# Performance work log

Hardware: AMD Instinct MI355X
Metric: run time of the kernel (lower is better)

The kernel has to match this reference:

```python
import jax, jax.numpy as jnp
import numpy as np

B, S, D, T = 64, 128, 512, 64  # batch, encoder len, dim_model, longest_coor

def setup_inputs() -> dict:
    key = jax.random.key(0)
    ks = jax.random.split(key, 10)
    def rn(k, shape, s=0.02):
        return jax.random.normal(k, shape, dtype=jnp.float32) * s
    return dict(
        e_all=jax.random.normal(ks[0], (B, S, D), dtype=jnp.float32),
        e_last=jax.random.normal(ks[1], (1, B, D), dtype=jnp.float32),
        Wa_w=rn(ks[2], (D, D)), Wa_b=jnp.zeros((D,), jnp.float32),
        Ua_w=rn(ks[3], (D, D)), Ua_b=jnp.zeros((D,), jnp.float32),
        Va_w=rn(ks[4], (D, 1)), Va_b=jnp.zeros((1,), jnp.float32),
        W_ih=rn(ks[5], (3 * D, D + 3)),  # GRU input weights, input = cat(attn[D], coord[3])
        W_hh=rn(ks[6], (3 * D, D)),
        b_ih=jnp.zeros((3 * D,), jnp.float32),
        b_hh=jnp.zeros((3 * D,), jnp.float32),
        Wo_w=rn(ks[7], (D, 3)), Wo_b=jnp.zeros((3,), jnp.float32),
    )

def reference(e_all, e_last, Wa_w, Wa_b, Ua_w, Ua_b, Va_w, Va_b,
              W_ih, W_hh, b_ih, b_hh, Wo_w, Wo_b):
    # Ua(keys) is step-invariant: hoist out of the decode loop (same math).
    Uk = e_all @ Ua_w + Ua_b                      # [B,S,D]
    h0 = e_last[0]                                # [B,D]
    x0 = jnp.zeros((e_all.shape[0], 3), e_all.dtype)

    def step(carry, _):
        h, x = carry
        # Bahdanau attention: query = current hidden state
        q = h @ Wa_w + Wa_b                       # [B,D]
        scores = jnp.squeeze(jnp.tanh(q[:, None, :] + Uk) @ Va_w, -1) + Va_b  # [B,S]
        w = jax.nn.softmax(scores, axis=-1)       # [B,S]
        ctx = jnp.einsum('bs,bsd->bd', w, e_all)  # [B,D]
        # single-step GRU, input = cat(context, prev coord)
        gin = jnp.concatenate([ctx, x], axis=-1)  # [B,D+3]
        gi = gin @ W_ih.T + b_ih                  # [B,3D]
        gh = h @ W_hh.T + b_hh                    # [B,3D]
        gir, giz, gin_n = jnp.split(gi, 3, axis=-1)
        ghr, ghz, ghn = jnp.split(gh, 3, axis=-1)
        r = jax.nn.sigmoid(gir + ghr)
        z = jax.nn.sigmoid(giz + ghz)
        n = jnp.tanh(gin_n + r * ghn)
        h_new = (1.0 - z) * n + z * h             # [B,D]
        out = h_new @ Wo_w + Wo_b                 # [B,3]
        return (h_new, out), (out, w)

    (hT, _), (outs, attns) = jax.lax.scan(step, (h0, x0), None, length=T)
    d_outputs = jnp.transpose(outs, (1, 0, 2))    # [B,T,3]
    cross_attn = jnp.transpose(attns, (1, 0, 2))  # [B,T,S]
    return d_outputs, hT[None], cross_attn
```

## Files before the change

### kernel.cpp

```cpp
#include <hip/hip_runtime.h>

typedef unsigned int u32;
typedef unsigned long long u64;
typedef float f32x4 __attribute__((ext_vector_type(4)));
typedef short short8 __attribute__((ext_vector_type(8)));

#define OFF_UKB 0u
#define OFF_ECB 8388608u
#define OFF_QX  16777216u
#define OFF_EX  17563648u
#define G_BYTES 73728u

#define OFF_OUT_HT  12288u
#define OFF_OUT_ATT 45056u

#define NBLK 192
#define NTHR 512
#define DYN_LDS 145408
#define PREP_LDS 36864

__device__ __forceinline__ float fast_rcp(float x) { return __builtin_amdgcn_rcpf(x); }
__device__ __forceinline__ float tanh5(float x) {
    float e = __expf(2.f * x);
    return 1.f - 2.f * fast_rcp(e + 1.f);
}
__device__ __forceinline__ float sigm_f(float x) { return fast_rcp(1.f + __expf(-x)); }

__device__ __forceinline__ u32 packbf2(float a, float b) {
    u32 ua = __float_as_uint(a); ua += 0x7FFFu + ((ua >> 16) & 1u);
    u32 ub = __float_as_uint(b); ub += 0x7FFFu + ((ub >> 16) & 1u);
    return (ua >> 16) | (ub & 0xFFFF0000u);
}
__device__ __forceinline__ float2 unpackbf2(u32 u) {
    return make_float2(__uint_as_float(u << 16), __uint_as_float(u & 0xFFFF0000u));
}
__device__ __forceinline__ float bf16hi(float x, float& lo) {
    u32 u = __float_as_uint(x); u += 0x7FFFu + ((u >> 16) & 1u); u &= 0xFFFF0000u;
    const float h = __uint_as_float(u); lo = x - h; return h;
}

__device__ __forceinline__ u64 cload64(const u64* p) {
    return __hip_atomic_load(p, __ATOMIC_RELAXED, __HIP_MEMORY_SCOPE_AGENT);
}
__device__ __forceinline__ void cstore64(u64* p, u64 v) {
    __hip_atomic_store(p, v, __ATOMIC_RELAXED, __HIP_MEMORY_SCOPE_AGENT);
}
__device__ __forceinline__ u32 cload32(const u32* p) {
    return __hip_atomic_load(p, __ATOMIC_RELAXED, __HIP_MEMORY_SCOPE_AGENT);
}
__device__ __forceinline__ void cstore32(u32* p, u32 v) {
    __hip_atomic_store(p, v, __ATOMIC_RELAXED, __HIP_MEMORY_SCOPE_AGENT);
}

union U8 { u32 u[4]; uint4 q; short8 s; };

__global__ __launch_bounds__(256) void prep_kernel(
    const float* __restrict__ e_all, const float* __restrict__ e_last,
    const float* __restrict__ Ua_w,  const float* __restrict__ Ua_b,
    float* __restrict__ ws)
{
    extern __shared__ char pls[];
    u32* Ahi = (u32*)pls;
    u32* Alo = Ahi + 64 * 36;
    u32* Bhi = Alo + 64 * 36;
    u32* Blo = Bhi + 64 * 36;

    u32* UKB = (u32*)((char*)ws + OFF_UKB);

    const int blk = blockIdx.x, tid = threadIdx.x;
    const int gtid = blk * 256 + tid, gstride = 1024 * 256;

    for (int i = gtid; i < 5120; i += gstride) {
        const int g = i / 1280, j = i - g * 1280;
        ((u32*)((char*)ws + OFF_EX + (size_t)g * G_BYTES + 65536))[j] = 0u;
    }
    for (int i = gtid; i < 8192; i += gstride) {
        const int g = i >> 11, i2 = i & 2047;
        const float* ep = e_last + ((size_t)(g * 16 + (i2 >> 7)) * 512) + 4 * (i2 & 127);
        u64* HX = (u64*)((char*)ws + OFF_EX + (size_t)g * G_BYTES);
        HX[i2] = (u64)packbf2(ep[0], ep[1]) | ((u64)packbf2(ep[2], ep[3]) << 32);
    }

    const int r0 = (blk >> 3) * 64, c0 = (blk & 7) * 64;
    const int lane = tid & 63, wv = tid >> 6;
    const int mn = lane & 15, quad = lane >> 4;

    f32x4 acc[4];
    #pragma unroll
    for (int rg = 0; rg < 4; ++rg) acc[rg] = (f32x4){0.f, 0.f, 0.f, 0.f};

    for (int ks = 0; ks < 8; ++ks) {
        if (ks) __syncthreads();
        for (int i = tid; i < 1024; i += 256) {
            const int row = i >> 4, q4i = i & 15;
            const float4 e = *(const float4*)(e_all + (size_t)(r0 + row) * 512 + ks * 64 + 4 * q4i);
            float l0, l1, l2, l3;
            const float h0 = bf16hi(e.x, l0), h1 = bf16hi(e.y, l1);
            const float h2 = bf16hi(e.z, l2), h3 = bf16hi(e.w, l3);
            Ahi[row * 36 + 2 * q4i]     = packbf2(h0, h1);
            Ahi[row * 36 + 2 * q4i + 1] = packbf2(h2, h3);
            Alo[row * 36 + 2 * q4i]     = packbf2(l0, l1);
            Alo[row * 36 + 2 * q4i + 1] = packbf2(l2, l3);
        }
        for (int i = tid; i < 2048; i += 256) {
            const int col = i & 63, kp = i >> 6;
            const float b0 = Ua_w[(size_t)(ks * 64 + 2 * kp) * 512 + c0 + col];
            const float b1 = Ua_w[(size_t)(ks * 64 + 2 * kp + 1) * 512 + c0 + col];
            float l0, l1;
            const float h0 = bf16hi(b0, l0), h1 = bf16hi(b1, l1);
            Bhi[col * 36 + kp] = packbf2(h0, h1);
            Blo[col * 36 + kp] = packbf2(l0, l1);
        }
        __syncthreads();
        #pragma unroll
        for (int kb = 0; kb < 2; ++kb) {
            const int fo = kb * 16 + quad * 4;
            U8 bh, bl;
            bh.q = *(const uint4*)(Bhi + (wv * 16 + mn) * 36 + fo);
            bl.q = *(const uint4*)(Blo + (wv * 16 + mn) * 36 + fo);
            #pragma unroll
            for (int rg = 0; rg < 4; ++rg) {
                U8 ah, al;
                ah.q = *(const uint4*)(Ahi + (rg * 16 + mn) * 36 + fo);
                al.q = *(const uint4*)(Alo + (rg * 16 + mn) * 36 + fo);
                acc[rg] = __builtin_amdgcn_mfma_f32_16x16x32_bf16(al.s, bh.s, acc[rg], 0, 0, 0);
                acc[rg] = __builtin_amdgcn_mfma_f32_16x16x32_bf16(ah.s, bl.s, acc[rg], 0, 0, 0);
                acc[rg] = __builtin_amdgcn_mfma_f32_16x16x32_bf16(ah.s, bh.s, acc[rg], 0, 0, 0);
            }
        }
    }
    const int col = c0 + wv * 16 + mn;
    const float bias = Ua_b[col];
    #pragma unroll
    for (int rg = 0; rg < 4; ++rg) {
        #pragma unroll
        for (int reg = 0; reg < 4; ++reg) {
            const float v = acc[rg][reg] + bias;
            const float v1 = __shfl_down(v, 1);
            if (!(mn & 1))
                UKB[(size_t)(r0 + rg * 16 + quad * 4 + reg) * 256 + (col >> 1)] = packbf2(v, v1);
        }
    }
}

__global__ __launch_bounds__(512, 1) void decode_kernel(
    const float* __restrict__ e_all,
    const float* __restrict__ e_last,
    const float* __restrict__ Wa_w,  const float* __restrict__ Wa_b,
    const float* __restrict__ Va_w,
    const float* __restrict__ W_ih,  const float* __restrict__ W_hh,
    const float* __restrict__ b_ih,  const float* __restrict__ b_hh,
    const float* __restrict__ Wo_w,  const float* __restrict__ Wo_b,
    float* __restrict__ out, float* __restrict__ ws)
{
    extern __shared__ char smraw[];

    const u32* UKB = (const u32*)((char*)ws + OFF_UKB);

    const int tid = threadIdx.x;
    const int bi  = blockIdx.x;
    const int g   = bi / 48, r = bi % 48;
    const int lane = tid & 63, wv = tid >> 6;

    char* gbase = (char*)ws + OFF_EX + (size_t)g * G_BYTES;
    u64* HX = (u64*)gbase;
    u64* CX = (u64*)(gbase + 32768);
    u32* FH = (u32*)(gbase + 65536);
    u32* FC = (u32*)(gbase + 67584);
    u32* FQ = (u32*)(gbase + 68608);

    if (r < 16) {
        const int bl = r, b = g * 16 + bl;
        u32*   EuL  = (u32*)smraw;
        float* eq_s = (float*)(smraw + 131072);
        float* w_s  = (float*)(smraw + 133120);
        float* red  = (float*)(smraw + 133632);
        float* psq  = (float*)(smraw + 133696);

        const u64* QXR = (const u64*)((char*)ws + OFF_QX + (size_t)g * 65536);

        {
            const uint4* src = (const uint4*)(UKB + (size_t)b * 32768);
            uint4* dst = (uint4*)EuL;
            #pragma unroll
            for (int i = 0; i < 16; ++i) {
                uint4 u = src[tid + 512 * i];
                float2 p;
                p = unpackbf2(u.x); u.x = packbf2(__expf(2.f * p.x), __expf(2.f * p.y));
                p = unpackbf2(u.y); u.y = packbf2(__expf(2.f * p.x), __expf(2.f * p.y));
                p = unpackbf2(u.z); u.z = packbf2(__expf(2.f * p.x), __expf(2.f * p.y));
                p = unpackbf2(u.w); u.w = packbf2(__expf(2.f * p.x), __expf(2.f * p.y));
                dst[tid + 512 * i] = u;
            }
        }
        uint2 ereg[32];
        {
            const int dq = tid & 127, sg = tid >> 7;
            const float* ep = e_all + (size_t)b * 65536;
            #pragma unroll
            for (int si = 0; si < 32; ++si) {
                const float4 e = *(const float4*)(ep + (size_t)(sg * 32 + si) * 512 + 4 * dq);
                ereg[si] = make_uint2(packbf2(e.x, e.y), packbf2(e.z, e.w));
            }
        }
        const int kl = lane & 15;
        float4 va2a[4], va2b[4];
        float vaSum = 0.f;
        #pragma unroll
        for (int it = 0; it < 4; ++it) {
            const float4 a  = *(const float4*)(Va_w + (it * 16 + kl) * 8);
            const float4 b2 = *(const float4*)(Va_w + (it * 16 + kl) * 8 + 4);
            vaSum += a.x + a.y + a.z + a.w + b2.x + b2.y + b2.z + b2.w;
            va2a[it] = make_float4(-2.f * a.x,  -2.f * a.y,  -2.f * a.z,  -2.f * a.w);
            va2b[it] = make_float4(-2.f * b2.x, -2.f * b2.y, -2.f * b2.z, -2.f * b2.w);
        }
        __syncthreads();

        for (int t = 0; t < 64; ++t) {
            const int slot = t & 1;
            u64* CxS = CX + slot * 2048;
            const u64* QxS = QXR + slot * 4096;

            if (tid < 256) {
                if (lane < 8) {
                    const u32* f = FQ + (wv * 8 + lane) * 16;
                    while (cload32(f) < (u32)(t + 1)) {}
                }
                const u64 v = cload64(QxS + bl * 256 + tid);
                const float q0 = __uint_as_float((u32)v);
                const float q1 = __uint_as_float((u32)(v >> 32));
                ((float2*)eq_s)[tid] = make_float2(__expf(2.f * q0), __expf(2.f * q1));
            }
            __syncthreads();

            {
                float4 eqa[4], eqb[4];
                const float4* q4 = (const float4*)eq_s;
                #pragma unroll
                for (int it = 0; it < 4; ++it) {
                    eqa[it] = q4[(it * 16 + kl) * 2];  eqb[it] = q4[(it * 16 + kl) * 2 + 1];
                }
                const int sbase = wv * 16 + (lane >> 4);
                #pragma unroll
                for (int sg = 0; sg < 4; ++sg) {
                    const int s = sbase + sg * 4;
                    const uint4* uk4 = (const uint4*)EuL + (size_t)s * 64;
                    float acc = vaSum;
                    #pragma unroll
                    for (int it = 0; it < 4; ++it) {
                        const uint4 u = uk4[it * 16 + kl];
                        const float2 u0 = unpackbf2(u.x), u1 = unpackbf2(u.y);
                        const float2 u2 = unpackbf2(u.z), u3 = unpackbf2(u.w);
                        acc = fmaf(va2a[it].x, fast_rcp(fmaf(eqa[it].x, u0.x, 1.f)), acc);
                        acc = fmaf(va2a[it].y, fast_rcp(fmaf(eqa[it].y, u0.y, 1.f)), acc);
                        acc = fmaf(va2a[it].z, fast_rcp(fmaf(eqa[it].z, u1.x, 1.f)), acc);
                        acc = fmaf(va2a[it].w, fast_rcp(fmaf(eqa[it].w, u1.y, 1.f)), acc);
                        acc = fmaf(va2b[it].x, fast_rcp(fmaf(eqb[it].x, u2.x, 1.f)), acc);
                        acc = fmaf(va2b[it].y, fast_rcp(fmaf(eqb[it].y, u2.y, 1.f)), acc);
                        acc = fmaf(va2b[it].z, fast_rcp(fmaf(eqb[it].z, u3.x, 1.f)), acc);
                        acc = fmaf(va2b[it].w, fast_rcp(fmaf(eqb[it].w, u3.y, 1.f)), acc);
                    }
                    acc += __shfl_xor(acc, 1); acc += __shfl_xor(acc, 2);
                    acc += __shfl_xor(acc, 4); acc += __shfl_xor(acc, 8);
                    if (kl == 0) w_s[s] = __expf(acc);
                }
            }
            __syncthreads();

            if (tid < 64) {
                float sm = w_s[tid] + w_s[tid + 64];
                #pragma unroll
                for (int off = 32; off > 0; off >>= 1) sm += __shfl_down(sm, off);
                if (tid == 0) red[1] = fast_rcp(sm);
            }
            {
                const int dq = tid & 127, sg = tid >> 7;
                float4 a = {0.f, 0.f, 0.f, 0.f};
                #pragma unroll
                for (int si = 0; si < 32; ++si) {
                    const float wgt = w_s[sg * 32 + si];
                    const float2 e0 = unpackbf2(ereg[si].x), e1 = unpackbf2(ereg[si].y);
                    a.x = fmaf(wgt, e0.x, a.x);
                    a.y = fmaf(wgt, e0.y, a.y);
                    a.z = fmaf(wgt, e1.x, a.z);
                    a.w = fmaf(wgt, e1.y, a.w);
                }
                ((float4*)psq)[sg * 128 + dq] = a;
            }
            __syncthreads();
            if (tid < 128) {
                const float rn = red[1];
                const float4* p4 = (const float4*)psq;
                float4 a = p4[tid], b2 = p4[128 + tid], c2 = p4[256 + tid], d2 = p4[384 + tid];
                const float rx = (a.x + b2.x + c2.x + d2.x) * rn;
                const float ry = (a.y + b2.y + c2.y + d2.y) * rn;
                const float rz = (a.z + b2.z + c2.z + d2.z) * rn;
                const float rw = (a.w + b2.w + c2.w + d2.w) * rn;
                cstore64(CxS + bl * 128 + tid,
                         (u64)packbf2(rx, ry) | ((u64)packbf2(rz, rw) << 32));
            }
            __syncthreads();
            if (tid == 0) cstore32(FC + bl * 16, (u32)(t + 1));
            else if (tid >= 128 && tid < 256)
                out[OFF_OUT_ATT + ((size_t)b * 64 + t) * 128 + (tid - 128)] = w_s[tid - 128] * red[1];
        }
    } else {
        const int idx = r - 16, d0 = idx * 16;
        u32*   hbu  = (u32*)smraw;
        u32*   cbu  = (u32*)(smraw + 16640);
        float* gh_s = (float*)(smraw + 33280);
        float* gi_s = (float*)(smraw + 36352);
        float* x_s  = (float*)(smraw + 39424);
        float* wx_s = (float*)(smraw + 39616);
        float* wo_s = (float*)(smraw + 40192);

        u64* QXW = (u64*)((char*)ws + OFF_QX + (size_t)g * 65536);

        const int mn = lane & 15, quad = lane >> 4;

        short8 bfrag[16];
        float qbias = 0.f;
        if (wv < 3) {
            const float* wrow = W_hh + (size_t)(wv * 512 + d0 + mn) * 512;
            #pragma unroll
            for (int kb = 0; kb < 16; ++kb) {
                const int k0 = kb * 32 + quad * 8;
                U8 tpk;
                #pragma unroll
                for (int c = 0; c < 4; ++c)
                    tpk.u[c] = packbf2(wrow[k0 + 2 * c], wrow[k0 + 2 * c + 1]);
                bfrag[kb] = tpk.s;
            }
        } else if (wv < 6) {
            const float* wrow = W_ih + (size_t)((wv - 3) * 512 + d0 + mn) * 515;
            #pragma unroll
            for (int kb = 0; kb < 16; ++kb) {
                const int k0 = kb * 32 + quad * 8;
                U8 tpk;
                #pragma unroll
                for (int c = 0; c < 4; ++c)
                    tpk.u[c] = packbf2(wrow[k0 + 2 * c], wrow[k0 + 2 * c + 1]);
                bfrag[kb] = tpk.s;
            }
        } else if (wv == 6) {
            #pragma unroll
            for (int kb = 0; kb < 16; ++kb) {
                const int k0 = kb * 32 + quad * 8;
                U8 tpk;
                #pragma unroll
                for (int c = 0; c < 4; ++c)
                    tpk.u[c] = packbf2(Wa_w[(size_t)(k0 + 2 * c) * 512 + d0 + mn],
                                       Wa_w[(size_t)(k0 + 2 * c + 1) * 512 + d0 + mn]);
                bfrag[kb] = tpk.s;
            }
            qbias = Wa_b[d0 + mn];
        }
        if (tid < 144) {
            const int dd = tid / 9, rem = tid - dd * 9, g3 = rem / 3, c = rem - g3 * 3;
            wx_s[tid] = W_ih[(size_t)(g3 * 512 + d0 + dd) * 515 + 512 + c];
        }
        for (int i = tid; i < 1536; i += 512) wo_s[i] = Wo_w[i];
        if (tid < 3) wo_s[1536 + tid] = Wo_b[tid];

        const int gb = tid >> 4, gd = tid & 15;
        float hold = 0.f, bih[3], bhh[3];
        if (tid < 256) {
            hold = e_last[(size_t)(g * 16 + gb) * 512 + d0 + gd];
            #pragma unroll
            for (int g3 = 0; g3 < 3; ++g3) {
                bih[g3] = b_ih[g3 * 512 + d0 + gd];
                bhh[g3] = b_hh[g3 * 512 + d0 + gd];
            }
        }

        for (int t = 0; t < 64; ++t) {
            const int slot = t & 1;
            const u64* HxS = HX + slot * 2048;
            const u64* CxS = CX + slot * 2048;
            u64* HxW = HX + ((t + 1) & 1) * 2048;

            if (lane < 16) {
                const u32* f = FH + ((wv & 1) * 16 + lane) * 16;
                while (cload32(f) < (u32)t) {}
            }
            #pragma unroll
            for (int u = 0; u < 4; ++u) {
                const int i = tid + 512 * u;
                const u64 v = cload64(HxS + i);
                *(u64*)(hbu + (i >> 7) * 260 + (i & 127) * 2) = v;
            }
            __syncthreads();

            if (wv < 3) {
                f32x4 c = {0.f, 0.f, 0.f, 0.f};
                #pragma unroll
                for (int kb = 0; kb < 16; ++kb) {
                    U8 a; a.q = *(const uint4*)(hbu + mn * 260 + kb * 16 + quad * 4);
                    c = __builtin_amdgcn_mfma_f32_16x16x32_bf16(a.s, bfrag[kb], c, 0, 0, 0);
                }
                #pragma unroll
                for (int reg = 0; reg < 4; ++reg)
                    gh_s[((quad * 4 + reg) * 16 + mn) * 3 + wv] = c[reg];
            } else if (wv < 6) {
                if (lane < 16) { const u32* f = FC + lane * 16; while (cload32(f) < (u32)(t + 1)) {} }
                const int thr = (wv - 3) * 64 + lane;
                for (int i = thr; i < 2048; i += 192) {
                    const u64 v = cload64(CxS + i);
                    *(u64*)(cbu + (i >> 7) * 260 + (i & 127) * 2) = v;
                }
            } else if (wv == 6) {
                f32x4 c = {0.f, 0.f, 0.f, 0.f};
                #pragma unroll
                for (int kb = 0; kb < 16; ++kb) {
                    U8 a; a.q = *(const uint4*)(hbu + mn * 260 + kb * 16 + quad * 4);
                    c = __builtin_amdgcn_mfma_f32_16x16x32_bf16(a.s, bfrag[kb], c, 0, 0, 0);
                }
                u64* QxW = QXW + slot * 4096;
                #pragma unroll
                for (int reg = 0; reg < 4; ++reg) {
                    const float q0 = c[reg] + qbias;
                    const float q1 = __shfl_down(q0, 1);
                    if ((mn & 1) == 0)
                        cstore64(QxW + (size_t)(quad * 4 + reg) * 256 + idx * 8 + (mn >> 1),
                                 (u64)__float_as_uint(q0) | ((u64)__float_as_uint(q1) << 32));
                }
                asm volatile("s_waitcnt vmcnt(0)" ::: "memory");
                if (lane == 0) cstore32(FQ + idx * 16, (u32)(t + 1));
            } else {
                const int tt = tid - 448, cb = tt >> 2, kl = tt & 3;
                if (t > 0) {
                    float a0 = 0.f, a1 = 0.f, a2 = 0.f;
                    #pragma unroll 4
                    for (int c = 0; c < 64; ++c) {
                        const int p = kl * 64 + c;
                        const float2 hv = unpackbf2(hbu[cb * 260 + p]);
                        const float* w0 = wo_s + 2 * p * 3;
                        a0 = fmaf(hv.x, w0[0], fmaf(hv.y, w0[3], a0));
                        a1 = fmaf(hv.x, w0[1], fmaf(hv.y, w0[4], a1));
                        a2 = fmaf(hv.x, w0[2], fmaf(hv.y, w0[5], a2));
                    }
                    a0 += __shfl_xor(a0, 1); a1 += __shfl_xor(a1, 1); a2 += __shfl_xor(a2, 1);
                    a0 += __shfl_xor(a0, 2); a1 += __shfl_xor(a1, 2); a2 += __shfl_xor(a2, 2);
                    if (kl == 0) {
                        x_s[cb * 3 + 0] = a0 + wo_s[1536];
                        x_s[cb * 3 + 1] = a1 + wo_s[1537];
                        x_s[cb * 3 + 2] = a2 + wo_s[1538];
                    }
                } else if (tt < 48) x_s[tt] = 0.f;
            }
            __syncthreads();

            if (wv >= 3 && wv < 6) {
                f32x4 c = {0.f, 0.f, 0.f, 0.f};
                #pragma unroll
                for (int kb = 0; kb < 16; ++kb) {
                    U8 a; a.q = *(const uint4*)(cbu + mn * 260 + kb * 16 + quad * 4);
                    c = __builtin_amdgcn_mfma_f32_16x16x32_bf16(a.s, bfrag[kb], c, 0, 0, 0);
                }
                #pragma unroll
                for (int reg = 0; reg < 4; ++reg)
                    gi_s[((quad * 4 + reg) * 16 + mn) * 3 + (wv - 3)] = c[reg];
            } else if (idx == 0 && t > 0 && tid < 48) {
                out[((size_t)(g * 16 + tid / 3) * 64 + (t - 1)) * 3 + tid % 3] = x_s[tid];
            }
            __syncthreads();

            if (tid < 256) {
                const int ob = (gb * 16 + gd) * 3;
                const float x0 = x_s[gb * 3 + 0], x1 = x_s[gb * 3 + 1], x2 = x_s[gb * 3 + 2];
                const float giR = gi_s[ob + 0] + bih[0]
                                + x0 * wx_s[gd * 9 + 0] + x1 * wx_s[gd * 9 + 1] + x2 * wx_s[gd * 9 + 2];
                const float giZ = gi_s[ob + 1] + bih[1]
                                + x0 * wx_s[gd * 9 + 3] + x1 * wx_s[gd * 9 + 4] + x2 * wx_s[gd * 9 + 5];
                const float giN = gi_s[ob + 2] + bih[2]
                                + x0 * wx_s[gd * 9 + 6] + x1 * wx_s[gd * 9 + 7] + x2 * wx_s[gd * 9 + 8];
                const float ghR = gh_s[ob + 0] + bhh[0];
                const float ghZ = gh_s[ob + 1] + bhh[1];
                const float ghN = gh_s[ob + 2] + bhh[2];
                const float rg = sigm_f(giR + ghR);
                const float zg = sigm_f(giZ + ghZ);
                const float ng = tanh5(giN + rg * ghN);
                const float hnew = (1.f - zg) * ng + zg * hold;
                hold = hnew;
                const float s1 = __shfl_down(hnew, 1);
                const float s2 = __shfl_down(hnew, 2);
                const float s3 = __shfl_down(hnew, 3);
                if ((gd & 3) == 0)
                    cstore64(HxW + gb * 128 + ((d0 + gd) >> 2),
                             (u64)packbf2(hnew, s1) | ((u64)packbf2(s2, s3) << 32));
                if (t == 63)
                    out[OFF_OUT_HT + (size_t)(g * 16 + gb) * 512 + d0 + gd] = hnew;
            }
            __syncthreads();
            if (tid == 0) cstore32(FH + idx * 16, (u32)(t + 1));
        }

        if (tid < 32) { const u32* f = FH + tid * 16; while (cload32(f) < 64u) {} }
        __syncthreads();
        #pragma unroll
        for (int u = 0; u < 4; ++u) {
            const int i = tid + 512 * u;
            const u64 v = cload64(HX + i);
            *(u64*)(hbu + (i >> 7) * 260 + (i & 127) * 2) = v;
        }
        __syncthreads();
        if (wv >= 6) {
            const int tt = tid - 384, cb = tt >> 3, kl = tt & 7;
            float a0 = 0.f, a1 = 0.f, a2 = 0.f;
            #pragma unroll 4
            for (int c = 0; c < 32; ++c) {
                const int p = kl * 32 + c;
                const float2 hv = unpackbf2(hbu[cb * 260 + p]);
                const float* w0 = wo_s + 2 * p * 3;
                a0 = fmaf(hv.x, w0[0], fmaf(hv.y, w0[3], a0));
                a1 = fmaf(hv.x, w0[1], fmaf(hv.y, w0[4], a1));
                a2 = fmaf(hv.x, w0[2], fmaf(hv.y, w0[5], a2));
            }
            a0 += __shfl_xor(a0, 1); a1 += __shfl_xor(a1, 1); a2 += __shfl_xor(a2, 1);
            a0 += __shfl_xor(a0, 2); a1 += __shfl_xor(a1, 2); a2 += __shfl_xor(a2, 2);
            a0 += __shfl_xor(a0, 4); a1 += __shfl_xor(a1, 4); a2 += __shfl_xor(a2, 4);
            if (kl == 0) {
                x_s[cb * 3 + 0] = a0 + wo_s[1536];
                x_s[cb * 3 + 1] = a1 + wo_s[1537];
                x_s[cb * 3 + 2] = a2 + wo_s[1538];
            }
        }
        __syncthreads();
        if (idx == 0 && tid < 48)
            out[((size_t)(g * 16 + tid / 3) * 64 + 63) * 3 + tid % 3] = x_s[tid];
    }
}

extern "C" void kernel_launch(void* const* d_in, const int* in_sizes, int n_in,
                              void* d_out, int out_size, void* d_ws, size_t ws_size,
                              hipStream_t stream) {
    const float* e_all  = (const float*)d_in[0];
    const float* e_last = (const float*)d_in[1];
    const float* Wa_w   = (const float*)d_in[2];
    const float* Wa_b   = (const float*)d_in[3];
    const float* Ua_w   = (const float*)d_in[4];
    const float* Ua_b   = (const float*)d_in[5];
    const float* Va_w   = (const float*)d_in[6];
    const float* W_ih   = (const float*)d_in[8];
    const float* W_hh   = (const float*)d_in[9];
    const float* b_ih   = (const float*)d_in[10];
    const float* b_hh   = (const float*)d_in[11];
    const float* Wo_w   = (const float*)d_in[12];
    const float* Wo_b   = (const float*)d_in[13];
    float* outp = (float*)d_out;
    float* ws   = (float*)d_ws;

    hipFuncSetAttribute((const void*)prep_kernel,
                        hipFuncAttributeMaxDynamicSharedMemorySize, PREP_LDS);
    hipFuncSetAttribute((const void*)decode_kernel,
                        hipFuncAttributeMaxDynamicSharedMemorySize, DYN_LDS);

    hipLaunchKernelGGL(prep_kernel, dim3(1024), dim3(256), PREP_LDS, stream,
                       e_all, e_last, Ua_w, Ua_b, ws);

    void* args[] = { (void*)&e_all, (void*)&e_last, (void*)&Wa_w, (void*)&Wa_b,
                     (void*)&Va_w,
                     (void*)&W_ih, (void*)&W_hh, (void*)&b_ih, (void*)&b_hh,
                     (void*)&Wo_w, (void*)&Wo_b, (void*)&outp, (void*)&ws };
    hipError_t err = hipLaunchCooperativeKernel((void*)decode_kernel, dim3(NBLK), dim3(NTHR),
                                                args, DYN_LDS, stream);
    if (err != hipSuccess) {
        hipLaunchKernelGGL(decode_kernel, dim3(NBLK), dim3(NTHR), DYN_LDS, stream,
                           e_all, e_last, Wa_w, Wa_b, Va_w,
                           W_ih, W_hh, b_ih, b_hh, Wo_w, Wo_b, outp, ws);
    }
}
```

Before: 955.3 us.

## Fuse Ua key projection into decode kernel and drop prep launch

```diff
diff --git a/kernel.cpp b/kernel.cpp
--- a/kernel.cpp
+++ b/kernel.cpp
@@ -1,12 +1,11 @@
 #include <hip/hip_runtime.h>
+#include <hip/hip_cooperative_groups.h>
 
 typedef unsigned int u32;
 typedef unsigned long long u64;
 typedef float f32x4 __attribute__((ext_vector_type(4)));
 typedef short short8 __attribute__((ext_vector_type(8)));
 
-#define OFF_UKB 0u
-#define OFF_ECB 8388608u
 #define OFF_QX  16777216u
 #define OFF_EX  17563648u
 #define G_BYTES 73728u
@@ -17,7 +16,6 @@
 #define NBLK 192
 #define NTHR 512
 #define DYN_LDS 145408
-#define PREP_LDS 36864
 
 __device__ __forceinline__ float fast_rcp(float x) { return __builtin_amdgcn_rcpf(x); }
 __device__ __forceinline__ float tanh5(float x) {
@@ -54,92 +52,14 @@
 
 union U8 { u32 u[4]; uint4 q; short8 s; };
 
-__global__ __launch_bounds__(256) void prep_kernel(
-    const float* __restrict__ e_all, const float* __restrict__ e_last,
-    const float* __restrict__ Ua_w,  const float* __restrict__ Ua_b,
-    float* __restrict__ ws)
-{
-    extern __shared__ char pls[];
-    u32* Ahi = (u32*)pls;
-    u32* Alo = Ahi + 64 * 36;
-    u32* Bhi = Alo + 64 * 36;
-    u32* Blo = Bhi + 64 * 36;
-
-    u32* UKB = (u32*)((char*)ws + OFF_UKB);
-
-    const int blk = blockIdx.x, tid = threadIdx.x;
-    const int gtid = blk * 256 + tid, gstride = 1024 * 256;
-
-    for (int i = gtid; i < 5120; i += gstride) {
-        const int g = i / 1280, j = i - g * 1280;
-        ((u32*)((char*)ws + OFF_EX + (size_t)g * G_BYTES + 65536))[j] = 0u;
-    }
-    for (int i = gtid; i < 8192; i += gstride) {
-        const int g = i >> 11, i2 = i & 2047;
-        const float* ep = e_last + ((size_t)(g * 16 + (i2 >> 7)) * 512) + 4 * (i2 & 127);
-        u64* HX = (u64*)((char*)ws + OFF_EX + (size_t)g * G_BYTES);
-        HX[i2] = (u64)packbf2(ep[0], ep[1]) | ((u64)packbf2(ep[2], ep[3]) << 32);
-    }
-
-    const int r0 = (blk >> 3) * 64, c0 = (blk & 7) * 64;
-    const int lane = tid & 63, wv = tid >> 6;
-    const int mn = lane & 15, quad = lane >> 4;
-
-    f32x4 acc[4];
-    #pragma unroll
-    for (int rg = 0; rg < 4; ++rg) acc[rg] = (f32x4){0.f, 0.f, 0.f, 0.f};
-
-    for (int ks = 0; ks < 8; ++ks) {
-        if (ks) __syncthreads();
-        for (int i = tid; i < 1024; i += 256) {
-            const int row = i >> 4, q4i = i & 15;
-            const float4 e = *(const float4*)(e_all + (size_t)(r0 + row) * 512 + ks * 64 + 4 * q4i);
-            float l0, l1, l2, l3;
-            const float h0 = bf16hi(e.x, l0), h1 = bf16hi(e.y, l1);
-            const float h2 = bf16hi(e.z, l2), h3 = bf16hi(e.w, l3);
-            Ahi[row * 36 + 2 * q4i]     = packbf2(h0, h1);
-            Ahi[row * 36 + 2 * q4i + 1] = packbf2(h2, h3);
-            Alo[row * 36 + 2 * q4i]     = packbf2(l0, l1);
-            Alo[row * 36 + 2 * q4i + 1] = packbf2(l2, l3);
-        }
-        for (int i = tid; i < 2048; i += 256) {
-            const int col = i & 63, kp = i >> 6;
-            const float b0 = Ua_w[(size_t)(ks * 64 + 2 * kp) * 512 + c0 + col];
-            const float b1 = Ua_w[(size_t)(ks * 64 + 2 * kp + 1) * 512 + c0 + col];
-            float l0, l1;
-            const float h0 = bf16hi(b0, l0), h1 = bf16hi(b1, l1);
-            Bhi[col * 36 + kp] = packbf2(h0, h1);
-            Blo[col * 36 + kp] = packbf2(l0, l1);
-        }
-        __syncthreads();
-        #pragma unroll
-        for (int kb = 0; kb < 2; ++kb) {
-            const int fo = kb * 16 + quad * 4;
-            U8 bh, bl;
-            bh.q = *(const uint4*)(Bhi + (wv * 16 + mn) * 36 + fo);
-            bl.q = *(const uint4*)(Blo + (wv * 16 + mn) * 36 + fo);
-            #pragma unroll
-            for (int rg = 0; rg < 4; ++rg) {
-                U8 ah, al;
-                ah.q = *(const uint4*)(Ahi + (rg * 16 + mn) * 36 + fo);
-                al.q = *(const uint4*)(Alo + (rg * 16 + mn) * 36 + fo);
-                acc[rg] = __builtin_amdgcn_mfma_f32_16x16x32_bf16(al.s, bh.s, acc[rg], 0, 0, 0);
-                acc[rg] = __builtin_amdgcn_mfma_f32_16x16x32_bf16(ah.s, bl.s, acc[rg], 0, 0, 0);
-                acc[rg] = __builtin_amdgcn_mfma_f32_16x16x32_bf16(ah.s, bh.s, acc[rg], 0, 0, 0);
-            }
-        }
-    }
-    const int col = c0 + wv * 16 + mn;
-    const float bias = Ua_b[col];
-    #pragma unroll
-    for (int rg = 0; rg < 4; ++rg) {
-        #pragma unroll
-        for (int reg = 0; reg < 4; ++reg) {
-            const float v = acc[rg][reg] + bias;
-            const float v1 = __shfl_down(v, 1);
-            if (!(mn & 1))
-                UKB[(size_t)(r0 + rg * 16 + quad * 4 + reg) * 256 + (col >> 1)] = packbf2(v, v1);
-        }
+__global__ __launch_bounds__(256) void flagzero_kernel(float* __restrict__ ws) {
+    const int tid = threadIdx.x;
+    for (int i = tid; i < 320; i += 256) {
+        const int g = i / 80, j = i - g * 80;
+        char* gb = (char*)ws + OFF_EX + (size_t)g * G_BYTES;
+        if (j < 32)      ((u32*)(gb + 65536))[j * 16] = 0u;
+        else if (j < 48) ((u32*)(gb + 67584))[(j - 32) * 16] = 0u;
+        else             ((u32*)(gb + 68608))[(j - 48) * 16] = 0u;
     }
 }
 
@@ -148,14 +68,13 @@
     const float* __restrict__ e_last,
     const float* __restrict__ Wa_w,  const float* __restrict__ Wa_b,
     const float* __restrict__ Va_w,
+    const float* __restrict__ Ua_w,  const float* __restrict__ Ua_b,
     const float* __restrict__ W_ih,  const float* __restrict__ W_hh,
     const float* __restrict__ b_ih,  const float* __restrict__ b_hh,
     const float* __restrict__ Wo_w,  const float* __restrict__ Wo_b,
-    float* __restrict__ out, float* __restrict__ ws)
+    float* __restrict__ out, float* __restrict__ ws, int fused)
 {
     extern __shared__ char smraw[];
-
-    const u32* UKB = (const u32*)((char*)ws + OFF_UKB);
 
     const int tid = threadIdx.x;
     const int bi  = blockIdx.x;
@@ -168,6 +87,15 @@
     u32* FH = (u32*)(gbase + 65536);
     u32* FC = (u32*)(gbase + 67584);
     u32* FQ = (u32*)(gbase + 68608);
+
+    if (fused) {
+        if (tid == 0) {
+            if (r < 16) cstore32(FC + r * 16, 0u);
+            else { cstore32(FH + (r - 16) * 16, 0u); cstore32(FQ + (r - 16) * 16, 0u); }
+        }
+        __threadfence();
+        cooperative_groups::this_grid().sync();
+    }
 
     if (r < 16) {
         const int bl = r, b = g * 16 + bl;
@@ -178,21 +106,92 @@
         float* psq  = (float*)(smraw + 133696);
 
         const u64* QXR = (const u64*)((char*)ws + OFF_QX + (size_t)g * 65536);
+        const int mn = lane & 15, quad = lane >> 4;
 
         {
-            const uint4* src = (const uint4*)(UKB + (size_t)b * 32768);
-            uint4* dst = (uint4*)EuL;
-            #pragma unroll
-            for (int i = 0; i < 16; ++i) {
-                uint4 u = src[tid + 512 * i];
-                float2 p;
-                p = unpackbf2(u.x); u.x = packbf2(__expf(2.f * p.x), __expf(2.f * p.y));
-                p = unpackbf2(u.y); u.y = packbf2(__expf(2.f * p.x), __expf(2.f * p.y));
-                p = unpackbf2(u.z); u.z = packbf2(__expf(2.f * p.x), __expf(2.f * p.y));
-                p = unpackbf2(u.w); u.w = packbf2(__expf(2.f * p.x), __expf(2.f * p.y));
-                dst[tid + 512 * i] = u;
-            }
-        }
+            u32* Ahi = EuL;
+            u32* Alo = Ahi + 4096;
+            u32* Bhi = Alo + 4096;
+            u32* Blo = Bhi + 4096;
+            const float* eb = e_all + (size_t)b * 65536;
+
+            auto run_chunk = [&](int cc, f32x4* acc) {
+                #pragma unroll
+                for (int ct = 0; ct < 8; ++ct) acc[ct] = (f32x4){0.f, 0.f, 0.f, 0.f};
+                for (int kc = 0; kc < 8; ++kc) {
+                    __syncthreads();
+                    for (int i = tid; i < 2048; i += 512) {
+                        const int row = i >> 4, q4 = i & 15;
+                        const float4 e = *(const float4*)(eb + (size_t)row * 512 + kc * 64 + 4 * q4);
+                        float l0, l1, l2, l3;
+                        const float h0 = bf16hi(e.x, l0), h1 = bf16hi(e.y, l1);
+                        const float h2 = bf16hi(e.z, l2), h3 = bf16hi(e.w, l3);
+                        const int sw = (row & 7) << 2;
+                        const int k0 = 2 * q4, k1 = 2 * q4 + 1;
+                        const int a0 = row * 32 + (((k0 & ~3) ^ sw) | (k0 & 3));
+                        const int a1 = row * 32 + (((k1 & ~3) ^ sw) | (k1 & 3));
+                        Ahi[a0] = packbf2(h0, h1); Ahi[a1] = packbf2(h2, h3);
+                        Alo[a0] = packbf2(l0, l1); Alo[a1] = packbf2(l2, l3);
+                    }
+                    for (int i = tid; i < 4096; i += 512) {
+                        const int col = i & 127, kp = i >> 7;
+                        const float b0 = Ua_w[(size_t)(kc * 64 + 2 * kp) * 512 + cc * 128 + col];
+                        const float b1 = Ua_w[(size_t)(kc * 64 + 2 * kp + 1) * 512 + cc * 128 + col];
+                        float l0, l1;
+                        const float h0 = bf16hi(b0, l0), h1 = bf16hi(b1, l1);
+                        const int sw = (col & 7) << 2;
+                        const int ad = col * 32 + (((kp & ~3) ^ sw) | (kp & 3));
+                        Bhi[ad] = packbf2(h0, h1);
+                        Blo[ad] = packbf2(l0, l1);
+                    }
+                    __syncthreads();
+                    #pragma unroll
+                    for (int kb = 0; kb < 2; ++kb) {
+                        const int arow = wv * 16 + mn;
+                        const int fo = (kb * 16 + quad * 4) ^ ((mn & 7) << 2);
+                        U8 ah, al;
+                        ah.q = *(const uint4*)(Ahi + arow * 32 + fo);
+                        al.q = *(const uint4*)(Alo + arow * 32 + fo);
+                        #pragma unroll
+                        for (int ct = 0; ct < 8; ++ct) {
+                            const int bcol = ct * 16 + mn;
+                            U8 bh, bl;
+                            bh.q = *(const uint4*)(Bhi + bcol * 32 + fo);
+                            bl.q = *(const uint4*)(Blo + bcol * 32 + fo);
+                            acc[ct] = __builtin_amdgcn_mfma_f32_16x16x32_bf16(al.s, bh.s, acc[ct], 0, 0, 0);
+                            acc[ct] = __builtin_amdgcn_mfma_f32_16x16x32_bf16(ah.s, bl.s, acc[ct], 0, 0, 0);
+                            acc[ct] = __builtin_amdgcn_mfma_f32_16x16x32_bf16(ah.s, bh.s, acc[ct], 0, 0, 0);
+                        }
+                    }
+                }
+            };
+            auto write_chunk = [&](int cc, f32x4* acc) {
+                #pragma unroll
+                for (int ct = 0; ct < 8; ++ct) {
+                    const float bias = Ua_b[cc * 128 + ct * 16 + mn];
+                    #pragma unroll
+                    for (int reg = 0; reg < 4; ++reg) {
+                        float lo_;
+                        const float ukr = bf16hi(acc[ct][reg] + bias, lo_);
+                        const float ev  = __expf(2.f * ukr);
+                        const float ev1 = __shfl_down(ev, 1);
+                        if (!(mn & 1)) {
+                            const int s = wv * 16 + quad * 4 + reg;
+                            EuL[cc * 8192 + s * 64 + ct * 8 + (mn >> 1)] = packbf2(ev, ev1);
+                        }
+                    }
+                }
+            };
+            f32x4 accA[8], accB[8];
+            run_chunk(3, accA); __syncthreads(); write_chunk(3, accA);
+            run_chunk(2, accA); __syncthreads(); write_chunk(2, accA);
+            run_chunk(1, accA);
+            run_chunk(0, accB);
+            __syncthreads();
+            write_chunk(1, accA);
+            write_chunk(0, accB);
+        }
+
         uint2 ereg[32];
         {
             const int dq = tid & 127, sg = tid >> 7;
@@ -240,15 +239,15 @@
                 for (int it = 0; it < 4; ++it) {
                     eqa[it] = q4[(it * 16 + kl) * 2];  eqb[it] = q4[(it * 16 + kl) * 2 + 1];
                 }
+                const uint4* ub = (const uint4*)EuL;
                 const int sbase = wv * 16 + (lane >> 4);
                 #pragma unroll
                 for (int sg = 0; sg < 4; ++sg) {
                     const int s = sbase + sg * 4;
-                    const uint4* uk4 = (const uint4*)EuL + (size_t)s * 64;
                     float acc = vaSum;
                     #pragma unroll
                     for (int it = 0; it < 4; ++it) {
-                        const uint4 u = uk4[it * 16 + kl];
+                        const uint4 u = ub[it * 2048 + s * 16 + kl];
                         const float2 u0 = unpackbf2(u.x), u1 = unpackbf2(u.y);
                         const float2 u2 = unpackbf2(u.z), u3 = unpackbf2(u.w);
                         acc = fmaf(va2a[it].x, fast_rcp(fmaf(eqa[it].x, u0.x, 1.f)), acc);
@@ -379,15 +378,25 @@
             const u64* CxS = CX + slot * 2048;
             u64* HxW = HX + ((t + 1) & 1) * 2048;
 
-            if (lane < 16) {
-                const u32* f = FH + ((wv & 1) * 16 + lane) * 16;
-                while (cload32(f) < (u32)t) {}
-            }
-            #pragma unroll
-            for (int u = 0; u < 4; ++u) {
-                const int i = tid + 512 * u;
-                const u64 v = cload64(HxS + i);
-                *(u64*)(hbu + (i >> 7) * 260 + (i & 127) * 2) = v;
+            if (t > 0) {
+                if (lane < 16) {
+                    const u32* f = FH + ((wv & 1) * 16 + lane) * 16;
+                    while (cload32(f) < (u32)t) {}
+                }
+                #pragma unroll
+                for (int u = 0; u < 4; ++u) {
+                    const int i = tid + 512 * u;
+                    const u64 v = cload64(HxS + i);
+                    *(u64*)(hbu + (i >> 7) * 260 + (i & 127) * 2) = v;
+                }
+            } else {
+                #pragma unroll
+                for (int u = 0; u < 4; ++u) {
+                    const int i = tid + 512 * u;
+                    const float4 ev = *(const float4*)(e_last + (size_t)(g * 16 + (i >> 7)) * 512 + 4 * (i & 127));
+                    *(u64*)(hbu + (i >> 7) * 260 + (i & 127) * 2) =
+                        (u64)packbf2(ev.x, ev.y) | ((u64)packbf2(ev.z, ev.w) << 32);
+                }
             }
             __syncthreads();
 
@@ -550,23 +559,21 @@
     float* outp = (float*)d_out;
     float* ws   = (float*)d_ws;
 
-    hipFuncSetAttribute((const void*)prep_kernel,
-                        hipFuncAttributeMaxDynamicSharedMemorySize, PREP_LDS);
     hipFuncSetAttribute((const void*)decode_kernel,
                         hipFuncAttributeMaxDynamicSharedMemorySize, DYN_LDS);
 
-    hipLaunchKernelGGL(prep_kernel, dim3(1024), dim3(256), PREP_LDS, stream,
-                       e_all, e_last, Ua_w, Ua_b, ws);
-
+    int fused = 1;
     void* args[] = { (void*)&e_all, (void*)&e_last, (void*)&Wa_w, (void*)&Wa_b,
-                     (void*)&Va_w,
+                     (void*)&Va_w, (void*)&Ua_w, (void*)&Ua_b,
                      (void*)&W_ih, (void*)&W_hh, (void*)&b_ih, (void*)&b_hh,
-                     (void*)&Wo_w, (void*)&Wo_b, (void*)&outp, (void*)&ws };
+                     (void*)&Wo_w, (void*)&Wo_b, (void*)&outp, (void*)&ws,
+                     (void*)&fused };
     hipError_t err = hipLaunchCooperativeKernel((void*)decode_kernel, dim3(NBLK), dim3(NTHR),
                                                 args, DYN_LDS, stream);
     if (err != hipSuccess) {
+        hipLaunchKernelGGL(flagzero_kernel, dim3(1), dim3(256), 0, stream, ws);
         hipLaunchKernelGGL(decode_kernel, dim3(NBLK), dim3(NTHR), DYN_LDS, stream,
-                           e_all, e_last, Wa_w, Wa_b, Va_w,
-                           W_ih, W_hh, b_ih, b_hh, Wo_w, Wo_b, outp, ws);
+                           e_all, e_last, Wa_w, Wa_b, Va_w, Ua_w, Ua_b,
+                           W_ih, W_hh, b_ih, b_hh, Wo_w, Wo_b, outp, ws, 0);
     }
 }
```

After: 1.117 ms. +16.9%, slower.

## Replace per-block Q ready flags with step-tagged Q values polled directly

Applied to the files above, without the earlier changes.

```diff
diff --git a/kernel.cpp b/kernel.cpp
--- a/kernel.cpp
+++ b/kernel.cpp
@@ -6,7 +6,6 @@
 typedef short short8 __attribute__((ext_vector_type(8)));
 
 #define OFF_UKB 0u
-#define OFF_ECB 8388608u
 #define OFF_QX  16777216u
 #define OFF_EX  17563648u
 #define G_BYTES 73728u
@@ -74,6 +73,8 @@
         const int g = i / 1280, j = i - g * 1280;
         ((u32*)((char*)ws + OFF_EX + (size_t)g * G_BYTES + 65536))[j] = 0u;
     }
+    for (int i = gtid; i < 65536; i += gstride)
+        ((u64*)((char*)ws + OFF_QX))[i] = 0ull;
     for (int i = gtid; i < 8192; i += gstride) {
         const int g = i >> 11, i2 = i & 2047;
         const float* ep = e_last + ((size_t)(g * 16 + (i2 >> 7)) * 512) + 4 * (i2 & 127);
@@ -167,7 +168,6 @@
     u64* CX = (u64*)(gbase + 32768);
     u32* FH = (u32*)(gbase + 65536);
     u32* FC = (u32*)(gbase + 67584);
-    u32* FQ = (u32*)(gbase + 68608);
 
     if (r < 16) {
         const int bl = r, b = g * 16 + bl;
@@ -177,7 +177,7 @@
         float* red  = (float*)(smraw + 133632);
         float* psq  = (float*)(smraw + 133696);
 
-        const u64* QXR = (const u64*)((char*)ws + OFF_QX + (size_t)g * 65536);
+        const u64* QXR = (const u64*)((char*)ws + OFF_QX + (size_t)g * 131072u);
 
         {
             const uint4* src = (const uint4*)(UKB + (size_t)b * 32768);
@@ -218,18 +218,16 @@
 
         for (int t = 0; t < 64; ++t) {
             const int slot = t & 1;
+            const u32 tg = (u32)(t + 1);
             u64* CxS = CX + slot * 2048;
-            const u64* QxS = QXR + slot * 4096;
+            const u64* QxS = QXR + slot * 8192 + (size_t)bl * 512;
 
             if (tid < 256) {
-                if (lane < 8) {
-                    const u32* f = FQ + (wv * 8 + lane) * 16;
-                    while (cload32(f) < (u32)(t + 1)) {}
-                }
-                const u64 v = cload64(QxS + bl * 256 + tid);
-                const float q0 = __uint_as_float((u32)v);
-                const float q1 = __uint_as_float((u32)(v >> 32));
-                ((float2*)eq_s)[tid] = make_float2(__expf(2.f * q0), __expf(2.f * q1));
+                u64 v0 = cload64(QxS + 2 * tid), v1 = cload64(QxS + 2 * tid + 1);
+                while ((u32)(v0 >> 32) != tg) v0 = cload64(QxS + 2 * tid);
+                while ((u32)(v1 >> 32) != tg) v1 = cload64(QxS + 2 * tid + 1);
+                ((float2*)eq_s)[tid] = make_float2(__uint_as_float((u32)v0),
+                                                   __uint_as_float((u32)v1));
             }
             __syncthreads();
 
@@ -314,7 +312,7 @@
         float* wx_s = (float*)(smraw + 39616);
         float* wo_s = (float*)(smraw + 40192);
 
-        u64* QXW = (u64*)((char*)ws + OFF_QX + (size_t)g * 65536);
+        u64* QXW = (u64*)((char*)ws + OFF_QX + (size_t)g * 131072u);
 
         const int mn = lane & 15, quad = lane >> 4;
 
@@ -415,17 +413,15 @@
                     U8 a; a.q = *(const uint4*)(hbu + mn * 260 + kb * 16 + quad * 4);
                     c = __builtin_amdgcn_mfma_f32_16x16x32_bf16(a.s, bfrag[kb], c, 0, 0, 0);
                 }
-                u64* QxW = QXW + slot * 4096;
+                u64* QxW = QXW + slot * 8192;
+                const u64 tg64 = (u64)(u32)(t + 1) << 32;
                 #pragma unroll
                 for (int reg = 0; reg < 4; ++reg) {
                     const float q0 = c[reg] + qbias;
-                    const float q1 = __shfl_down(q0, 1);
-                    if ((mn & 1) == 0)
-                        cstore64(QxW + (size_t)(quad * 4 + reg) * 256 + idx * 8 + (mn >> 1),
-                                 (u64)__float_as_uint(q0) | ((u64)__float_as_uint(q1) << 32));
-                }
-                asm volatile("s_waitcnt vmcnt(0)" ::: "memory");
-                if (lane == 0) cstore32(FQ + idx * 16, (u32)(t + 1));
+                    const float e  = __expf(2.f * q0);
+                    cstore64(QxW + (size_t)(quad * 4 + reg) * 512 + d0 + mn,
+                             tg64 | (u64)__float_as_uint(e));
+                }
             } else {
                 const int tt = tid - 448, cb = tt >> 2, kl = tt & 3;
                 if (t > 0) {
```

Result: faster. 914.1 us (-4.3%).
